# Performance work log

Hardware: AMD Instinct MI355X
Metric: run time of the kernel (lower is better)

Reference implementation:

```python
import jax, jax.numpy as jnp
import numpy as np

C = 128   # channels / dim
NH = 4    # num heads
HD = C // NH
K = 5     # conv kernel size: t=int((log2(128)+1)/2)=4 -> k=5
P = 12    # patch size
GH = 8    # grid height/width (96/12)
NPATCH = GH * GH
FEAT = P * P * C


def _ln(x, g, b):
    m = jnp.mean(x, -1, keepdims=True)
    v = jnp.var(x, -1, keepdims=True)
    return (x - m) / jnp.sqrt(v + 1e-5) * g + b


def _conv1d(x, w, pad):
    return jax.lax.conv_general_dilated(x, w, (1,), [(pad, pad)], dimension_numbers=('NCH', 'OIH', 'NCH'))


def _pool(x, out):
    # exact adaptive avg pool when H % out == 0
    B, c, H, W = x.shape
    f = H // out
    return x.reshape(B, c, out, f, out, f).mean((3, 5))


def _bilinear_ac(x, out):
    # bilinear interpolate [B,C,H,H] -> [B,C,out,out], align_corners=True
    H = x.shape[2]
    cpos = jnp.arange(out) * (H - 1) / (out - 1)
    i0 = jnp.floor(cpos).astype(jnp.int32)
    i1 = jnp.minimum(i0 + 1, H - 1)
    w = (cpos - i0).astype(x.dtype)
    xh = x[:, :, i0, :] * (1 - w)[None, None, :, None] + x[:, :, i1, :] * w[None, None, :, None]
    return xh[:, :, :, i0] * (1 - w) + xh[:, :, :, i1] * w


def setup_inputs() -> dict:
    key = jax.random.key(0)
    ks = jax.random.split(key, 8)
    B = 16
    return {
        's1': jax.random.normal(ks[0], (B, C, 96, 96), jnp.float32),
        'o': jax.random.normal(ks[1], (B, C, 64, 64), jnp.float32),
        'index': jax.random.randint(ks[2], (4, 2), 0, 96),
        'pe_w': jax.random.normal(ks[3], (64, 64, K), jnp.float32) * 0.05,
        'bn_g': jnp.ones((64,), jnp.float32),
        'bn_b': jnp.zeros((64,), jnp.float32),
        'bn_m': jnp.zeros((64,), jnp.float32),
        'bn_v': jnp.ones((64,), jnp.float32),
        'lnx_g': jnp.ones((C,), jnp.float32),
        'lnx_b': jnp.zeros((C,), jnp.float32),
        'lny_g': jnp.ones((C,), jnp.float32),
        'lny_b': jnp.zeros((C,), jnp.float32),
        'qkv_w': jax.random.normal(ks[4], (3 * C, C), jnp.float32) * 0.02,
        'qkv_b': jnp.zeros((3 * C,), jnp.float32),
        'yv_w': jax.random.normal(ks[5], (C, C), jnp.float32) * 0.02,
        'yv_b': jnp.zeros((C,), jnp.float32),
        'proj_w': jax.random.normal(ks[6], (C, C), jnp.float32) * 0.02,
        'proj_b': jnp.zeros((C,), jnp.float32),
        'c1d_w': jax.random.normal(ks[7], (C, C, K), jnp.float32) * 0.05,
    }


def reference(s1, o, index, pe_w, bn_g, bn_b, bn_m, bn_v, lnx_g, lnx_b, lny_g, lny_b,
              qkv_w, qkv_b, yv_w, yv_b, proj_w, proj_b, c1d_w):
    B = s1.shape[0]
    pad = (K - 1) // 2
    # --- mask(s1): patch embedding, conv1d+BN(eval)+ReLU, selective-square mask ---
    # einops: b c (h p1) (w p2) -> b (h w) (p1 p2 c)
    x = s1.reshape(B, C, GH, P, GH, P).transpose(0, 2, 4, 3, 5, 1).reshape(B, NPATCH, FEAT)
    x = _conv1d(x, pe_w, pad)
    x = (x - bn_m[None, :, None]) / jnp.sqrt(bn_v + 1e-5)[None, :, None] * bn_g[None, :, None] + bn_b[None, :, None]
    x = jax.nn.relu(x)
    # mask: rows at center indices keep value (mul by 1), all other rows squared
    idxs = index[:, 0] // P * GH + index[:, 1] // P
    sel = jnp.zeros((NPATCH,), bool).at[idxs].set(True)
    x = x * jnp.where(sel[None, :, None], 1.0, x)
    # einops back: b (h w) (p1 p2 c) -> b c (h p1) (w p2), then pool to 32
    x = x.reshape(B, GH, GH, P, P, C).transpose(0, 5, 1, 3, 2, 4).reshape(B, C, 96, 96)
    short = _pool(x, 32)                                   # [B,C,32,32]
    # --- attention branch ---
    op = _pool(o, 32)
    N = 32 * 32
    of = _ln(op.reshape(B, C, N).transpose(0, 2, 1), lnx_g, lnx_b)   # [B,N,C]
    ori = short.reshape(B, C, N).transpose(0, 2, 1)
    sn = _ln(ori, lny_g, lny_b)
    qkv = (of @ qkv_w.T + qkv_b).reshape(B, N, 3, NH, HD).transpose(2, 0, 3, 1, 4)
    q, k, v = qkv[0], qkv[1], qkv[2]                       # each [B,H,N,D]
    yv = (sn @ yv_w.T + yv_b).reshape(B, N, NH, HD).transpose(0, 2, 1, 3)
    attn = jax.nn.softmax(jnp.einsum('bhnd,bhmd->bhnm', q, k) * HD ** -0.5, axis=-1)
    xv = v + jnp.einsum('bhnm,bhmd->bhnd', attn, yv)
    xv = xv.transpose(0, 2, 1, 3).reshape(B, N, C) @ proj_w.T + proj_b
    xv = (xv + ori).transpose(0, 2, 1)                     # [B,C,N]
    xv = xv + _conv1d(xv, c1d_w, pad)
    xv = xv.reshape(B, C, 32, 32)
    return _bilinear_ac(xv, 96)
```

## Files before the change

kernel.cpp:

```cpp
#include <hip/hip_runtime.h>

#define FEAT 18432

typedef __attribute__((ext_vector_type(8))) short short8;
typedef __attribute__((ext_vector_type(4))) float f32x4;

__device__ __forceinline__ float b2f(unsigned short s) {
  union { unsigned int u; float f; } v; v.u = ((unsigned int)s) << 16; return v.f;
}
__device__ __forceinline__ unsigned short f2bf(float x) {
  union { float f; unsigned int u; } v; v.f = x;
  unsigned int u = v.u;
  unsigned int r = (u + 0x7FFFu + ((u >> 16) & 1u)) >> 16;
  return (unsigned short)r;
}

__device__ __forceinline__ void gl_lds16(const void* g, void* l) {
  __builtin_amdgcn_global_load_lds(
      (const __attribute__((address_space(1))) unsigned int*)g,
      (__attribute__((address_space(3))) unsigned int*)l, 16, 0, 0);
}

__global__ __launch_bounds__(256) void k_transpose(const float* __restrict__ s1,
                                                   unsigned short* __restrict__ xT) {
  int c = blockIdx.x, b = blockIdx.y;
  __shared__ float lds[96 * 99];
  int t = threadIdx.x;
  const float* src = s1 + ((size_t)b * 128 + c) * 9216;
  for (int idx = t; idx < 2304; idx += 256) {
    float4 v = ((const float4*)src)[idx];
    int h = idx / 24, w0 = (idx - h * 24) * 4;
    float* p = lds + h * 99 + w0;
    p[0] = v.x; p[1] = v.y; p[2] = v.z; p[3] = v.w;
  }
  __syncthreads();
  unsigned short* dstb = xT + (size_t)b * FEAT * 64;
  int sw = c & 7;
  for (int idx = t; idx < 1152; idx += 256) {
    int p1p2 = idx >> 3, gh = idx & 7;
    int p1 = p1p2 / 12, p2 = p1p2 - p1 * 12;
    const float* row = lds + (gh * 12 + p1) * 99 + p2;
    uint4 u;
    u.x = f2bf(row[0])  | ((unsigned int)f2bf(row[12]) << 16);
    u.y = f2bf(row[24]) | ((unsigned int)f2bf(row[36]) << 16);
    u.z = f2bf(row[48]) | ((unsigned int)f2bf(row[60]) << 16);
    u.w = f2bf(row[72]) | ((unsigned int)f2bf(row[84]) << 16);
    int f = p1p2 * 128 + c;
    int pos = gh ^ sw;
    *(uint4*)(dstb + (size_t)f * 64 + pos * 8) = u;
  }
}

__global__ __launch_bounds__(256) void k_prep(const float* __restrict__ pe_w,
                                              unsigned short* __restrict__ wpk) {
  int oc0 = blockIdx.x * 8;
  for (int e = threadIdx.x; e < 2560; e += 256) {
    int oc = oc0 + e / 320;
    int kL = e - (e / 320) * 320;
    int ic = kL & 63, kk = kL >> 6;
    float v = pe_w[(oc * 64 + ic) * 5 + kk];
    int LC = kL >> 3;
    int pos = (LC & 56) | ((LC & 7) ^ (oc & 7));
    wpk[oc * 320 + (pos << 3) + (kL & 7)] = f2bf(v);
  }
}

__global__ __launch_bounds__(256) void k_prepcw(const float* __restrict__ cw,
                                                unsigned short* __restrict__ wch) {
  int e = blockIdx.x * 256 + threadIdx.x;
  int oc = e / 640, kl = e - (e / 640) * 640;
  int kk = kl >> 7, ic = kl & 127;
  float v = cw[(size_t)oc * 640 + ic * 5 + kk];
  int LC = kl >> 3;
  int pos = (LC & 120) | ((LC & 7) ^ (oc & 7));
  wch[(size_t)oc * 640 + pos * 8 + (kl & 7)] = f2bf(v);
}

__global__ __launch_bounds__(256) void k_prepw(const float* __restrict__ W,
                                               unsigned short* __restrict__ dst,
                                               int ncols) {
  int idx = blockIdx.x * 256 + threadIdx.x;
  if (idx >= ncols * 16) return;
  int n = idx >> 4, c = idx & 15;
  int slot = (c & 8) | ((c & 7) ^ (n & 7));
  const float* s = W + (size_t)n * 128 + c * 8;
  uint4 u;
  u.x = (unsigned int)f2bf(s[0]) | ((unsigned int)f2bf(s[1]) << 16);
  u.y = (unsigned int)f2bf(s[2]) | ((unsigned int)f2bf(s[3]) << 16);
  u.z = (unsigned int)f2bf(s[4]) | ((unsigned int)f2bf(s[5]) << 16);
  u.w = (unsigned int)f2bf(s[6]) | ((unsigned int)f2bf(s[7]) << 16);
  *(uint4*)(dst + (size_t)n * 128 + slot * 8) = u;
}

__global__ __launch_bounds__(256) void k_conv_pe(
    const unsigned short* __restrict__ xT, const unsigned short* __restrict__ wpk,
    const float* __restrict__ bn_g, const float* __restrict__ bn_b,
    const float* __restrict__ bn_m, const float* __restrict__ bn_v,
    const int* __restrict__ indexp, unsigned short* __restrict__ ym) {
  extern __shared__ char smem[];
  unsigned short* Wl = (unsigned short*)smem;
  unsigned short* xl = (unsigned short*)(smem + 40960);
  float* scf = (float*)(smem + 74240);
  float* shf = (float*)(smem + 74496);
  int*   sli = (int*)(smem + 74752);
  int t = threadIdx.x;
  int b = blockIdx.y;
  int blk_f0 = blockIdx.x << 9;
  int lane = t & 63, w = t >> 6;
  int n16 = lane & 15, q = lane >> 4;

  for (int j = 0; j < 10; ++j) {
    int seg = w * 10 + j;
    gl_lds16((const char*)wpk + (seg << 10) + lane * 16, (char*)Wl + (seg << 10));
  }
  if (t < 64) {
    float sc = bn_g[t] * rsqrtf(bn_v[t] + 1e-5f);
    scf[t] = sc;
    shf[t] = bn_b[t] - bn_m[t] * sc;
    int i0 = indexp[0] / 12 * 8 + indexp[1] / 12;
    int i1 = indexp[2] / 12 * 8 + indexp[3] / 12;
    int i2 = indexp[4] / 12 * 8 + indexp[5] / 12;
    int i3 = indexp[6] / 12 * 8 + indexp[7] / 12;
    sli[t] = (t == i0 || t == i1 || t == i2 || t == i3) ? 1 : 0;
  }

  const unsigned short* xb = xT + (size_t)b * FEAT * 64;
  const unsigned int* xbu = (const unsigned int*)xb;

  for (int wnd = 0; wnd < 2; ++wnd) {
    int F0 = blk_f0 + (wnd << 8);
    __syncthreads();
    int flA = (F0 == 0) ? 2 : 0;
    for (int j = 0; j < 8; ++j) {
      int seg = (w << 3) + j;
      int gRow = F0 - 2 + flA + (seg << 3);
      gl_lds16((const char*)xb + (size_t)gRow * 128 + lane * 16,
               (char*)xl + flA * 128 + (seg << 10));
    }
    if (t < 128) {
      int r0 = (flA == 2) ? 0 : 256;
      int fl = (t < 64) ? (r0 + (t >> 5)) : (258 + ((t >> 5) & 1));
      int j = t & 31;
      int f = F0 - 2 + fl;
      unsigned int v = 0;
      if (f >= 0 && f < FEAT) v = xbu[(size_t)f * 32 + j];
      ((unsigned int*)xl)[fl * 32 + j] = v;
    }
    __syncthreads();

    f32x4 acc[4][4];
#pragma unroll
    for (int mt = 0; mt < 4; ++mt)
#pragma unroll
      for (int nt = 0; nt < 4; ++nt) acc[mt][nt] = (f32x4){0.f, 0.f, 0.f, 0.f};

    int rowB = w * 64 + n16;
#pragma unroll
    for (int kk = 0; kk < 5; ++kk) {
      int swb = (n16 + kk + 6) & 7;
#pragma unroll
      for (int ih = 0; ih < 2; ++ih) {
        int ca = (ih << 2) | q;
        const unsigned short* Ap = Wl + kk * 64 + ((ca ^ (n16 & 7)) << 3) + n16 * 320;
        short8 a0 = *(const short8*)(Ap);
        short8 a1 = *(const short8*)(Ap + 16 * 320);
        short8 a2 = *(const short8*)(Ap + 32 * 320);
        short8 a3 = *(const short8*)(Ap + 48 * 320);
        const unsigned short* Bp = xl + ((ca ^ swb) << 3) + (rowB + kk) * 64;
        short8 b0 = *(const short8*)(Bp);
        short8 b1 = *(const short8*)(Bp + 16 * 64);
        short8 b2 = *(const short8*)(Bp + 32 * 64);
        short8 b3 = *(const short8*)(Bp + 48 * 64);
        acc[0][0] = __builtin_amdgcn_mfma_f32_16x16x32_bf16(a0, b0, acc[0][0], 0, 0, 0);
        acc[0][1] = __builtin_amdgcn_mfma_f32_16x16x32_bf16(a0, b1, acc[0][1], 0, 0, 0);
// ... 53 lines not shown
#pragma unroll
    for (int dy = 0; dy < 3; ++dy)
#pragma unroll
      for (int dx = 0; dx < 3; ++dx)
        s += b2f(src[pbase + (dy * 12 + dx) * 128]);
    float val = s * (1.f / 9.f);
    float su = val, q = val * val;
#pragma unroll
    for (int off = 32; off > 0; off >>= 1) {
      su += __shfl_xor(su, off, 64);
      q += __shfl_xor(q, off, 64);
    }
    if (l64 == 0) { red[wv * 2] = su; red[wv * 2 + 1] = q; }
    __syncthreads();
    float S = red[hr * 4 + 0] + red[hr * 4 + 2];
    float Q = red[hr * 4 + 1] + red[hr * 4 + 3];
    float mean = S * (1.f / 128.f);
    float var = Q * (1.f / 128.f) - mean * mean;
    float inv = rsqrtf(var + 1e-5f);
    int n = (oh0 + pg1) * 32 + ow0 + pg2;
    size_t base = ((size_t)b * 1024 + n) * 128;
    ori[base + c] = val;
    float lnv = (val - mean) * inv * g + bb;
    int ch = c >> 3;
    int slot = (ch & 8) | ((ch & 7) ^ (n & 7));
    snh[base + slot * 8 + (c & 7)] = f2bf(lnv);
    __syncthreads();
  }
}

__global__ __launch_bounds__(256) void k_poolo_ln(
    const float* __restrict__ o, const float* __restrict__ lng,
    const float* __restrict__ lnb, unsigned short* __restrict__ oflh) {
  int y = blockIdx.x, b = blockIdx.y;
  __shared__ float pl[128 * 33];
  int t = threadIdx.x;
  for (int idx = t; idx < 4096; idx += 256) {
    int xo = idx & 31, c = idx >> 5;
    const float* p = o + (((size_t)b * 128 + c) * 64 + 2 * y) * 64 + 2 * xo;
    float2 a = *(const float2*)p;
    float2 d = *(const float2*)(p + 64);
    pl[c * 33 + xo] = 0.25f * (a.x + a.y + d.x + d.y);
  }
  __syncthreads();
  int xo = t >> 3, l8 = t & 7;
  float v[16]; float s = 0.f, q = 0.f;
#pragma unroll
  for (int i = 0; i < 16; ++i) {
    float x = pl[(l8 * 16 + i) * 33 + xo];
    v[i] = x; s += x; q += x * x;
  }
#pragma unroll
  for (int off = 1; off < 8; off <<= 1) {
    s += __shfl_xor(s, off, 8);
    q += __shfl_xor(q, off, 8);
  }
  float mean = s * (1.f / 128.f);
  float var = q * (1.f / 128.f) - mean * mean;
  float inv = rsqrtf(var + 1e-5f);
  int n = y * 32 + xo;
  unsigned short* dst = oflh + ((size_t)b * 1024 + n) * 128;
  int m7 = n & 7;
#pragma unroll
  for (int h = 0; h < 2; ++h) {
    int c = l8 * 2 + h;
    int slot = (c & 8) | ((c & 7) ^ m7);
    uint4 u;
    float w0 = (v[h * 8 + 0] - mean) * inv * lng[c * 8 + 0] + lnb[c * 8 + 0];
    float w1 = (v[h * 8 + 1] - mean) * inv * lng[c * 8 + 1] + lnb[c * 8 + 1];
    float w2 = (v[h * 8 + 2] - mean) * inv * lng[c * 8 + 2] + lnb[c * 8 + 2];
    float w3 = (v[h * 8 + 3] - mean) * inv * lng[c * 8 + 3] + lnb[c * 8 + 3];
    float w4 = (v[h * 8 + 4] - mean) * inv * lng[c * 8 + 4] + lnb[c * 8 + 4];
    float w5 = (v[h * 8 + 5] - mean) * inv * lng[c * 8 + 5] + lnb[c * 8 + 5];
    float w6 = (v[h * 8 + 6] - mean) * inv * lng[c * 8 + 6] + lnb[c * 8 + 6];
    float w7 = (v[h * 8 + 7] - mean) * inv * lng[c * 8 + 7] + lnb[c * 8 + 7];
    u.x = (unsigned int)f2bf(w0) | ((unsigned int)f2bf(w1) << 16);
    u.y = (unsigned int)f2bf(w2) | ((unsigned int)f2bf(w3) << 16);
    u.z = (unsigned int)f2bf(w4) | ((unsigned int)f2bf(w5) << 16);
    u.w = (unsigned int)f2bf(w6) | ((unsigned int)f2bf(w7) << 16);
    *(uint4*)(dst + slot * 8) = u;
  }
}

__global__ __launch_bounds__(256) void k_gemm_mfma(
    const unsigned short* __restrict__ A, const unsigned short* __restrict__ W,
    const float* __restrict__ bias, float* __restrict__ out, int Ncols) {
  __shared__ unsigned short Al[128 * 128];
  __shared__ unsigned short Bl[64 * 128];
  int m0 = blockIdx.x << 7, n0 = blockIdx.y << 6;
  int t = threadIdx.x;
  int lane = t & 63, w = t >> 6;
  int n16 = lane & 15, q = lane >> 4;

  for (int j = 0; j < 8; ++j) {
    int seg = w * 8 + j;
    gl_lds16((const char*)A + (size_t)m0 * 256 + (seg << 10) + lane * 16,
             (char*)Al + (seg << 10));
  }
  for (int j = 0; j < 4; ++j) {
    int seg = w * 4 + j;
    gl_lds16((const char*)W + (size_t)n0 * 256 + (seg << 10) + lane * 16,
             (char*)Bl + (seg << 10));
  }
  __syncthreads();

  int wm = w >> 1, wn = w & 1;
  f32x4 acc[4][2];
#pragma unroll
  for (int mt = 0; mt < 4; ++mt)
#pragma unroll
    for (int nt = 0; nt < 2; ++nt) acc[mt][nt] = (f32x4){0.f, 0.f, 0.f, 0.f};

#pragma unroll
  for (int kf = 0; kf < 4; ++kf) {
    int ca = kf * 4 + q;
    int rA0 = wm * 64 + n16;
    const unsigned short* Ap0 = Al + (size_t)rA0 * 128;
    int slotA = (ca & 8) | ((ca & 7) ^ (rA0 & 7));
    short8 a0 = *(const short8*)(Ap0 + slotA * 8);
    short8 a1 = *(const short8*)(Ap0 + 16 * 128 + slotA * 8);
    short8 a2 = *(const short8*)(Ap0 + 32 * 128 + slotA * 8);
    short8 a3 = *(const short8*)(Ap0 + 48 * 128 + slotA * 8);
    int rB0 = wn * 32 + n16;
    const unsigned short* Bp0 = Bl + (size_t)rB0 * 128;
    int slotB = (ca & 8) | ((ca & 7) ^ (rB0 & 7));
    short8 b0 = *(const short8*)(Bp0 + slotB * 8);
    short8 b1 = *(const short8*)(Bp0 + 16 * 128 + slotB * 8);
    acc[0][0] = __builtin_amdgcn_mfma_f32_16x16x32_bf16(a0, b0, acc[0][0], 0, 0, 0);
    acc[0][1] = __builtin_amdgcn_mfma_f32_16x16x32_bf16(a0, b1, acc[0][1], 0, 0, 0);
    acc[1][0] = __builtin_amdgcn_mfma_f32_16x16x32_bf16(a1, b0, acc[1][0], 0, 0, 0);
    acc[1][1] = __builtin_amdgcn_mfma_f32_16x16x32_bf16(a1, b1, acc[1][1], 0, 0, 0);
    acc[2][0] = __builtin_amdgcn_mfma_f32_16x16x32_bf16(a2, b0, acc[2][0], 0, 0, 0);
    acc[2][1] = __builtin_amdgcn_mfma_f32_16x16x32_bf16(a2, b1, acc[2][1], 0, 0, 0);
    acc[3][0] = __builtin_amdgcn_mfma_f32_16x16x32_bf16(a3, b0, acc[3][0], 0, 0, 0);
    acc[3][1] = __builtin_amdgcn_mfma_f32_16x16x32_bf16(a3, b1, acc[3][1], 0, 0, 0);
  }

#pragma unroll
  for (int mt = 0; mt < 4; ++mt) {
#pragma unroll
    for (int i = 0; i < 4; ++i) {
      int m = m0 + wm * 64 + mt * 16 + q * 4 + i;
#pragma unroll
      for (int nt = 0; nt < 2; ++nt) {
        int n = n0 + wn * 32 + nt * 16 + n16;
        out[(size_t)m * Ncols + n] = acc[mt][nt][i] + bias[n];
      }
    }
  }
}

__global__ __launch_bounds__(256) void k_proj_mfma(
    const unsigned short* __restrict__ A, const unsigned short* __restrict__ W,
    const float* __restrict__ bias, const float* __restrict__ ori,
    float* __restrict__ xv2, unsigned short* __restrict__ xph) {
  __shared__ unsigned short Al[128 * 128];
  __shared__ unsigned short Bl[64 * 128];
  int m0 = blockIdx.x << 7, n0 = blockIdx.y << 6;
  int t = threadIdx.x;
  int lane = t & 63, w = t >> 6;
  int n16 = lane & 15, q = lane >> 4;

  for (int j = 0; j < 8; ++j) {
    int seg = w * 8 + j;
    gl_lds16((const char*)A + (size_t)m0 * 256 + (seg << 10) + lane * 16,
             (char*)Al + (seg << 10));
  }
  for (int j = 0; j < 4; ++j) {
    int seg = w * 4 + j;
    gl_lds16((const char*)W + (size_t)n0 * 256 + (seg << 10) + lane * 16,
             (char*)Bl + (seg << 10));
  }
  __syncthreads();

  int wm = w >> 1, wn = w & 1;
  f32x4 acc[4][2];
#pragma unroll
  for (int mt = 0; mt < 4; ++mt)
#pragma unroll
    for (int nt = 0; nt < 2; ++nt) acc[mt][nt] = (f32x4){0.f, 0.f, 0.f, 0.f};

#pragma unroll
  for (int kf = 0; kf < 4; ++kf) {
    int ca = kf * 4 + q;
    int rA0 = wm * 64 + n16;
    const unsigned short* Ap0 = Al + (size_t)rA0 * 128;
    int slotA = (ca & 8) | ((ca & 7) ^ (rA0 & 7));
    short8 a0 = *(const short8*)(Ap0 + slotA * 8);
    short8 a1 = *(const short8*)(Ap0 + 16 * 128 + slotA * 8);
    short8 a2 = *(const short8*)(Ap0 + 32 * 128 + slotA * 8);
    short8 a3 = *(const short8*)(Ap0 + 48 * 128 + slotA * 8);
    int rB0 = wn * 32 + n16;
    const unsigned short* Bp0 = Bl + (size_t)rB0 * 128;
    int slotB = (ca & 8) | ((ca & 7) ^ (rB0 & 7));
    short8 b0 = *(const short8*)(Bp0 + slotB * 8);
    short8 b1 = *(const short8*)(Bp0 + 16 * 128 + slotB * 8);
    acc[0][0] = __builtin_amdgcn_mfma_f32_16x16x32_bf16(a0, b0, acc[0][0], 0, 0, 0);
    acc[0][1] = __builtin_amdgcn_mfma_f32_16x16x32_bf16(a0, b1, acc[0][1], 0, 0, 0);
    acc[1][0] = __builtin_amdgcn_mfma_f32_16x16x32_bf16(a1, b0, acc[1][0], 0, 0, 0);
    acc[1][1] = __builtin_amdgcn_mfma_f32_16x16x32_bf16(a1, b1, acc[1][1], 0, 0, 0);
    acc[2][0] = __builtin_amdgcn_mfma_f32_16x16x32_bf16(a2, b0, acc[2][0], 0, 0, 0);
    acc[2][1] = __builtin_amdgcn_mfma_f32_16x16x32_bf16(a2, b1, acc[2][1], 0, 0, 0);
    acc[3][0] = __builtin_amdgcn_mfma_f32_16x16x32_bf16(a3, b0, acc[3][0], 0, 0, 0);
    acc[3][1] = __builtin_amdgcn_mfma_f32_16x16x32_bf16(a3, b1, acc[3][1], 0, 0, 0);
  }

  int bb = m0 >> 10;
  int nbase = (m0 & 1023) + wm * 64;
#pragma unroll
  for (int mt = 0; mt < 4; ++mt) {
    int nloc = nbase + mt * 16 + q * 4;
    const float* orow = ori + ((size_t)bb * 1024 + nloc) * 128;
#pragma unroll
    for (int nt = 0; nt < 2; ++nt) {
      int c = n0 + wn * 32 + nt * 16 + n16;
      float pb = bias[c];
      float4 vv;
      vv.x = acc[mt][nt][0] + pb + orow[c];
      vv.y = acc[mt][nt][1] + pb + orow[128 + c];
      vv.z = acc[mt][nt][2] + pb + orow[256 + c];
      vv.w = acc[mt][nt][3] + pb + orow[384 + c];
      *(float4*)(xv2 + ((size_t)bb * 128 + c) * 1024 + nloc) = vv;
      int ch = c >> 3, ce = c & 7;
#pragma unroll
      for (int i = 0; i < 4; ++i) {
        int nrow = nloc + i;
        int slot = (ch & 8) | ((ch & 7) ^ (nrow & 7));
        float val = (i == 0) ? vv.x : (i == 1) ? vv.y : (i == 2) ? vv.z : vv.w;
        xph[((size_t)bb * 1024 + nrow) * 128 + slot * 8 + ce] = f2bf(val);
      }
    }
  }
}

__global__ __launch_bounds__(256) void k_cvt(const float* __restrict__ qkv,
                                             const float* __restrict__ yv,
                                             unsigned short* __restrict__ qkb,
                                             unsigned short* __restrict__ vtb) {
  int nt = blockIdx.x, b = blockIdx.y;
  int n0 = nt << 6;
  int t = threadIdx.x;
  __shared__ unsigned short tl[64 * 132];
  const float* qb = qkv + ((size_t)b * 1024 + n0) * 384;
  for (int it = 0; it < 16; ++it) {
    int idx = it * 256 + t;
    int n = idx >> 6, c4 = idx & 63;
    float4 v = *(const float4*)(qb + (size_t)n * 384 + c4 * 4);
    int c = c4 << 2;
    int kind = c >> 7, h = (c >> 5) & 3, d = c & 31;
    uint2 u;
    u.x = (unsigned int)f2bf(v.x) | ((unsigned int)f2bf(v.y) << 16);
    u.y = (unsigned int)f2bf(v.z) | ((unsigned int)f2bf(v.w) << 16);
    *(uint2*)(qkb + ((((size_t)b * 4 + h) * 2 + kind) * 1024 + n0 + n) * 32 + d) = u;
  }
  const float* vb = yv + ((size_t)b * 1024 + n0) * 128;
  for (int it = 0; it < 8; ++it) {
    int idx = it * 256 + t;
    int n = idx >> 5, c4 = idx & 31;
    float4 v = *(const float4*)(vb + (size_t)n * 128 + c4 * 4);
    unsigned short* o = tl + n * 132 + c4 * 4;
    o[0] = f2bf(v.x); o[1] = f2bf(v.y); o[2] = f2bf(v.z); o[3] = f2bf(v.w);
  }
  __syncthreads();
  int c = t >> 1, half = t & 1;
  unsigned short* orow = vtb + (((size_t)b * 4 + (c >> 5)) * 32 + (c & 31)) * 1024 + n0 + half * 32;
#pragma unroll
  for (int k = 0; k < 4; ++k) {
    short8 pack;
#pragma unroll
    for (int j = 0; j < 8; ++j)
      pack[j] = (short)tl[(half * 32 + k * 8 + j) * 132 + c];
    *(short8*)(orow + k * 8) = pack;
  }
}

__global__ __launch_bounds__(256) void k_attn(const float* __restrict__ qkv,
                                              const unsigned short* __restrict__ qkb,
                                              const unsigned short* __restrict__ vtb,
                                              unsigned short* __restrict__ atth) {
  int qt = blockIdx.x, h = blockIdx.y, b = blockIdx.z;
  __shared__ unsigned short Qs[64 * 40];
  __shared__ unsigned short Ks[128 * 40];
  __shared__ unsigned short Vt[32 * 136];
  __shared__ unsigned short Pw[4 * 16 * 136];
  int t = threadIdx.x;
  int lane = t & 63, w = t >> 6;
  int quad = lane >> 4, l16 = lane & 15;
  const float* qbase = qkv + (size_t)b * 1024 * 384;
  const unsigned short* qrow = qkb + (((size_t)b * 4 + h) * 2 + 0) * 1024 * 32;
  const unsigned short* krow = qkb + (((size_t)b * 4 + h) * 2 + 1) * 1024 * 32;
  const unsigned short* vrow = vtb + ((size_t)b * 4 + h) * 32 * 1024;
  int q0 = qt << 6;
  int hd = h * 32;

  {
    int r = t >> 2, cq = t & 3;
    short8 v = *(const short8*)(qrow + (size_t)(q0 + r) * 32 + cq * 8);
    *(short8*)(Qs + r * 40 + cq * 8) = v;
  }
  __syncthreads();
  short8 aq = *(const short8*)(Qs + (w * 16 + l16) * 40 + quad * 8);

  f32x4 O[2];
  O[0] = (f32x4){0.f, 0.f, 0.f, 0.f};
  O[1] = (f32x4){0.f, 0.f, 0.f, 0.f};
  float mi0 = -1e30f, li0 = 0.f;
  unsigned short* Pme = Pw + w * (16 * 136);
  const float scl = 0.17677669529663688f;

  for (int ci = 0; ci < 8; ++ci) {
    __syncthreads();
    int kn0 = ci << 7;
#pragma unroll
    for (int it = 0; it < 2; ++it) {
      int idx = it * 256 + t;
      int r = idx >> 2, cq = idx & 3;
      short8 kv = *(const short8*)(krow + (size_t)(kn0 + r) * 32 + cq * 8);
      *(short8*)(Ks + r * 40 + cq * 8) = kv;
      int d = idx >> 4, cc = idx & 15;
      short8 vv = *(const short8*)(vrow + (size_t)d * 1024 + kn0 + cc * 8);
      *(short8*)(Vt + d * 136 + cc * 8) = vv;
    }
    __syncthreads();

    f32x4 S[8];
#pragma unroll
    for (int nt = 0; nt < 8; ++nt) S[nt] = (f32x4){0.f, 0.f, 0.f, 0.f};
    __builtin_amdgcn_s_setprio(1);
#pragma unroll
    for (int nt = 0; nt < 8; ++nt) {
      short8 bk = *(const short8*)(Ks + (nt * 16 + l16) * 40 + quad * 8);
      S[nt] = __builtin_amdgcn_mfma_f32_16x16x32_bf16(bk, aq, S[nt], 0, 0, 0);
    }
    __builtin_amdgcn_s_setprio(0);

    float mg[8];
#pragma unroll
    for (int nt = 0; nt < 8; ++nt)
      mg[nt] = fmaxf(fmaxf(S[nt][0], S[nt][1]), fmaxf(S[nt][2], S[nt][3]));
    float rmr = fmaxf(fmaxf(fmaxf(mg[0], mg[1]), fmaxf(mg[2], mg[3])),
                      fmaxf(fmaxf(mg[4], mg[5]), fmaxf(mg[6], mg[7])));
    float rm = rmr * scl;
    rm = fmaxf(rm, __shfl_xor(rm, 16));
    rm = fmaxf(rm, __shfl_xor(rm, 32));
    float nm = fmaxf(mi0, rm);
    float alpha = __expf(mi0 - nm);
    mi0 = nm;

    float pstot = 0.f;
    unsigned short* pwr = Pme + l16 * 136 + quad * 4;
#pragma unroll
    for (int nt = 0; nt < 8; ++nt) {
      float p0 = __expf(S[nt][0] * scl - nm);
      float p1 = __expf(S[nt][1] * scl - nm);
      float p2 = __expf(S[nt][2] * scl - nm);
      float p3 = __expf(S[nt][3] * scl - nm);
      pstot += (p0 + p1) + (p2 + p3);
      uint2 u;
      u.x = (unsigned int)f2bf(p0) | ((unsigned int)f2bf(p1) << 16);
      u.y = (unsigned int)f2bf(p2) | ((unsigned int)f2bf(p3) << 16);
      *(uint2*)(pwr + nt * 16) = u;
    }
    float ps = pstot;
    ps += __shfl_xor(ps, 16);
    ps += __shfl_xor(ps, 32);
    li0 = li0 * alpha + ps;

    float al0 = __shfl(alpha, quad * 4 + 0);
    float al1 = __shfl(alpha, quad * 4 + 1);
    float al2 = __shfl(alpha, quad * 4 + 2);
    float al3 = __shfl(alpha, quad * 4 + 3);
    O[0][0] *= al0; O[1][0] *= al0;
    O[0][1] *= al1; O[1][1] *= al1;
    O[0][2] *= al2; O[1][2] *= al2;
    O[0][3] *= al3; O[1][3] *= al3;

    __builtin_amdgcn_s_setprio(1);
#pragma unroll
    for (int kc = 0; kc < 4; ++kc) {
      short8 bv0 = *(const short8*)(Vt + l16 * 136 + kc * 32 + quad * 8);
      short8 bv1 = *(const short8*)(Vt + (16 + l16) * 136 + kc * 32 + quad * 8);
      short8 ap = *(const short8*)(Pme + l16 * 136 + kc * 32 + quad * 8);
      O[0] = __builtin_amdgcn_mfma_f32_16x16x32_bf16(ap, bv0, O[0], 0, 0, 0);
      O[1] = __builtin_amdgcn_mfma_f32_16x16x32_bf16(ap, bv1, O[1], 0, 0, 0);
    }
    __builtin_amdgcn_s_setprio(0);
  }

#pragma unroll
  for (int reg = 0; reg < 4; ++reg) {
    float lit = __shfl(li0, quad * 4 + reg);
    int n = q0 + w * 16 + quad * 4 + reg;
    float inv = 1.f / lit;
    size_t mrow = ((size_t)b * 1024 + n) * 128;
    int m7 = n & 7;
#pragma unroll
    for (int nt = 0; nt < 2; ++nt) {
      int dd = hd + nt * 16 + l16;
      float val = O[nt][reg] * inv + qbase[(size_t)n * 384 + 256 + dd];
      int ch = dd >> 3;
      int slot = (ch & 8) | ((ch & 7) ^ m7);
      atth[mrow + slot * 8 + (dd & 7)] = f2bf(val);
    }
  }
}

__global__ __launch_bounds__(256) void k_conv1d_mfma(
    const unsigned short* __restrict__ xph, const unsigned short* __restrict__ wch,
    const float* __restrict__ xv2, float* __restrict__ xv3) {
  extern __shared__ char cs[];
  unsigned short* Wl = (unsigned short*)cs;
  unsigned short* xl = (unsigned short*)(cs + 81920);
  int ntile = blockIdx.x, b = blockIdx.y, oh = blockIdx.z;
  int n0 = ntile << 7;
  int t = threadIdx.x, lane = t & 63, w = t >> 6;
  int n16 = lane & 15, q = lane >> 4;

  const unsigned short* wsrc = wch + (size_t)oh * 64 * 640;
  for (int j = 0; j < 20; ++j) {
    int seg = w * 20 + j;
    gl_lds16((const char*)wsrc + (seg << 10) + lane * 16, (char*)Wl + (seg << 10));
  }
  const unsigned short* xpb = xph + (size_t)b * 1024 * 128;
  for (int j = 0; j < 8; ++j) {
    int seg = w * 8 + j;
    gl_lds16((const char*)xpb + (size_t)n0 * 256 + (seg << 10) + lane * 16,
             (char*)xl + 512 + (seg << 10));
  }
  {
    int ri = t >> 6, j2 = t & 63;
    int j = (ri < 2) ? ri : (128 + ri);
    int n = n0 + j - 2;
    unsigned int v = 0;
    if (n >= 0 && n < 1024) v = ((const unsigned int*)xpb)[(size_t)n * 64 + j2];
    ((unsigned int*)xl)[j * 64 + j2] = v;
  }
  __syncthreads();

  f32x4 acc[4][2];
#pragma unroll
  for (int mt = 0; mt < 4; ++mt)
#pragma unroll
    for (int nt = 0; nt < 2; ++nt) acc[mt][nt] = (f32x4){0.f, 0.f, 0.f, 0.f};

  int nb = w * 32;
#pragma unroll
  for (int kk = 0; kk < 5; ++kk) {
    int swb = (n16 + kk + 6) & 7;
#pragma unroll
    for (int kf = 0; kf < 4; ++kf) {
      int ca = kf * 4 + q;
      int LC = kk * 16 + kf * 4 + q;
      int slotA = (LC & 120) | ((LC & 7) ^ (n16 & 7));
      const unsigned short* Ap = Wl + n16 * 640 + slotA * 8;
      short8 a0 = *(const short8*)(Ap);
      short8 a1 = *(const short8*)(Ap + 16 * 640);
      short8 a2 = *(const short8*)(Ap + 32 * 640);
      short8 a3 = *(const short8*)(Ap + 48 * 640);
      int slotB = (ca & 8) | ((ca & 7) ^ swb);
      const unsigned short* Bp = xl + (nb + n16 + kk) * 128 + slotB * 8;
      short8 b0 = *(const short8*)(Bp);
      short8 b1 = *(const short8*)(Bp + 16 * 128);
      acc[0][0] = __builtin_amdgcn_mfma_f32_16x16x32_bf16(a0, b0, acc[0][0], 0, 0, 0);
      acc[0][1] = __builtin_amdgcn_mfma_f32_16x16x32_bf16(a0, b1, acc[0][1], 0, 0, 0);
      acc[1][0] = __builtin_amdgcn_mfma_f32_16x16x32_bf16(a1, b0, acc[1][0], 0, 0, 0);
      acc[1][1] = __builtin_amdgcn_mfma_f32_16x16x32_bf16(a1, b1, acc[1][1], 0, 0, 0);
      acc[2][0] = __builtin_amdgcn_mfma_f32_16x16x32_bf16(a2, b0, acc[2][0], 0, 0, 0);
      acc[2][1] = __builtin_amdgcn_mfma_f32_16x16x32_bf16(a2, b1, acc[2][1], 0, 0, 0);
      acc[3][0] = __builtin_amdgcn_mfma_f32_16x16x32_bf16(a3, b0, acc[3][0], 0, 0, 0);
      acc[3][1] = __builtin_amdgcn_mfma_f32_16x16x32_bf16(a3, b1, acc[3][1], 0, 0, 0);
    }
  }

#pragma unroll
  for (int mt = 0; mt < 4; ++mt) {
#pragma unroll
    for (int i = 0; i < 4; ++i) {
      int oc = oh * 64 + mt * 16 + q * 4 + i;
      const float* res = xv2 + ((size_t)b * 128 + oc) * 1024;
      float* outp = xv3 + ((size_t)b * 128 + oc) * 1024;
#pragma unroll
      for (int nt = 0; nt < 2; ++nt) {
        int n = n0 + nb + nt * 16 + n16;
        outp[n] = acc[mt][nt][i] + res[n];
      }
    }
  }
}

__global__ __launch_bounds__(256) void k_bilinear(const float* __restrict__ xv3,
                                                  float* __restrict__ out) {
  int idx = blockIdx.x * 256 + threadIdx.x;
  int X = idx % 96;
  int t2 = idx / 96;
  int Y = t2 % 96;
  int bc = t2 / 96;
  const float* src = xv3 + (size_t)bc * 1024;
  const float r = 31.f / 95.f;
  float py = Y * r, px = X * r;
  int y0 = (int)py, x0 = (int)px;
  float wy = py - y0, wx = px - x0;
  int y1 = y0 < 31 ? y0 + 1 : 31, x1 = x0 < 31 ? x0 + 1 : 31;
  float a = src[y0 * 32 + x0], b_ = src[y0 * 32 + x1];
  float c_ = src[y1 * 32 + x0], d_ = src[y1 * 32 + x1];
  float t0 = a * (1.f - wy) + c_ * wy;
  float t1 = b_ * (1.f - wy) + d_ * wy;
  out[idx] = t0 * (1.f - wx) + t1 * wx;
}

extern "C" void kernel_launch(void* const* d_in, const int* in_sizes, int n_in,
                              void* d_out, int out_size, void* d_ws, size_t ws_size,
                              hipStream_t stream) {
  (void)in_sizes; (void)n_in; (void)out_size; (void)ws_size;
  const float* s1    = (const float*)d_in[0];
  const float* o     = (const float*)d_in[1];
  const int*   indx  = (const int*)d_in[2];
  const float* pe_w  = (const float*)d_in[3];
  const float* bn_g  = (const float*)d_in[4];
  const float* bn_b  = (const float*)d_in[5];
  const float* bn_m  = (const float*)d_in[6];
  const float* bn_v  = (const float*)d_in[7];
  const float* lnx_g = (const float*)d_in[8];
  const float* lnx_b = (const float*)d_in[9];
  const float* lny_g = (const float*)d_in[10];
  const float* lny_b = (const float*)d_in[11];
  const float* qkv_w = (const float*)d_in[12];
  const float* qkv_b = (const float*)d_in[13];
  const float* yv_w  = (const float*)d_in[14];
  const float* yv_b  = (const float*)d_in[15];
  const float* proj_w = (const float*)d_in[16];
  const float* proj_b = (const float*)d_in[17];
  const float* c1d_w  = (const float*)d_in[18];

  char* ws = (char*)d_ws;
  unsigned short* xTh = (unsigned short*)ws;
  unsigned short* ymh = (unsigned short*)(ws + 37748736);
  unsigned short* wpk = (unsigned short*)d_out;
  unsigned short* wch = (unsigned short*)((char*)d_out + 65536);
  unsigned short* wqkh = (unsigned short*)((char*)d_out + 458752);
  unsigned short* wyvh = (unsigned short*)((char*)d_out + 573440);
  unsigned short* wprh = (unsigned short*)((char*)d_out + 622592);
  float* ori  = (float*)ws;
  unsigned short* snh  = (unsigned short*)(ws + 8388608);
  unsigned short* oflh = (unsigned short*)(ws + 16777216);
  unsigned short* atth = (unsigned short*)(ws + 25165824);
  float* qkvb  = (float*)(ws + 37748736);
  float* yvbuf = (float*)(ws + 62914560);
  unsigned short* qkb = (unsigned short*)(ws + 16777216);
  unsigned short* vtb = (unsigned short*)(ws + 71303168);
  float* xv2   = (float*)(ws + 37748736);
  float* xv3   = (float*)(ws + 46137344);
  unsigned short* xph = (unsigned short*)(ws + 62914560);

  hipLaunchKernelGGL(k_prep, dim3(8), dim3(256), 0, stream, pe_w, wpk);
  hipLaunchKernelGGL(k_prepcw, dim3(320), dim3(256), 0, stream, c1d_w, wch);
  hipLaunchKernelGGL(k_prepw, dim3(24), dim3(256), 0, stream, qkv_w, wqkh, 384);
  hipLaunchKernelGGL(k_prepw, dim3(8), dim3(256), 0, stream, yv_w, wyvh, 128);
  hipLaunchKernelGGL(k_prepw, dim3(8), dim3(256), 0, stream, proj_w, wprh, 128);
  hipLaunchKernelGGL(k_transpose, dim3(128, 16), dim3(256), 0, stream, s1, xTh);
  hipLaunchKernelGGL(k_conv_pe, dim3(36, 16), dim3(256), 75008, stream,
                     xTh, wpk, bn_g, bn_b, bn_m, bn_v, indx, ymh);
  hipLaunchKernelGGL(k_pool9ln, dim3(64, 16), dim3(256), 0, stream, ymh, lny_g, lny_b, ori, snh);
  hipLaunchKernelGGL(k_poolo_ln, dim3(32, 16), dim3(256), 0, stream, o, lnx_g, lnx_b, oflh);
  hipLaunchKernelGGL(k_gemm_mfma, dim3(128, 6), dim3(256), 0, stream, oflh, wqkh, qkv_b, qkvb, 384);
  hipLaunchKernelGGL(k_gemm_mfma, dim3(128, 2), dim3(256), 0, stream, snh, wyvh, yv_b, yvbuf, 128);
  hipLaunchKernelGGL(k_cvt, dim3(16, 16), dim3(256), 0, stream, qkvb, yvbuf, qkb, vtb);
  hipLaunchKernelGGL(k_attn, dim3(16, 4, 16), dim3(256), 0, stream, qkvb, qkb, vtb, atth);
  hipLaunchKernelGGL(k_proj_mfma, dim3(128, 2), dim3(256), 0, stream, atth, wprh, proj_b, ori, xv2, xph);
  hipLaunchKernelGGL(k_conv1d_mfma, dim3(8, 16, 2), dim3(256), 115712, stream, xph, wch, xv2, xv3);
  hipLaunchKernelGGL(k_bilinear, dim3(73728), dim3(256), 0, stream, xv3, (float*)d_out);
}
```

Baseline: 345.6 us.

## Fuse bf16 conversion into QKV/YV GEMM epilogues and merge weight prep kernels

The QKV and YV GEMMs now write their results directly in the bf16 head-major layouts that attention consumes (Q/K packed per head, YV transposed per head), and V is written as a separate fp32 residual buffer. This removes the k_cvt kernel and its fp32 round trip through memory. The five weight-prep kernels are merged into one launch to cut launch overhead. In exchange, the epilogue stores become scattered 2-byte writes, which may coalesce poorly, and the workspace buffers are reassigned.

```diff
diff --git a/kernel.cpp b/kernel.cpp
--- a/kernel.cpp
+++ b/kernel.cpp
@@ -3,6 +3,7 @@
 #define FEAT 18432
 
 typedef __attribute__((ext_vector_type(8))) short short8;
+typedef __attribute__((ext_vector_type(4))) short short4t;
 typedef __attribute__((ext_vector_type(4))) float f32x4;
 
 __device__ __forceinline__ float b2f(unsigned short s) {
@@ -51,35 +52,10 @@
   }
 }
 
-__global__ __launch_bounds__(256) void k_prep(const float* __restrict__ pe_w,
-                                              unsigned short* __restrict__ wpk) {
-  int oc0 = blockIdx.x * 8;
-  for (int e = threadIdx.x; e < 2560; e += 256) {
-    int oc = oc0 + e / 320;
-    int kL = e - (e / 320) * 320;
-    int ic = kL & 63, kk = kL >> 6;
-    float v = pe_w[(oc * 64 + ic) * 5 + kk];
-    int LC = kL >> 3;
-    int pos = (LC & 56) | ((LC & 7) ^ (oc & 7));
-    wpk[oc * 320 + (pos << 3) + (kL & 7)] = f2bf(v);
-  }
-}
-
-__global__ __launch_bounds__(256) void k_prepcw(const float* __restrict__ cw,
-                                                unsigned short* __restrict__ wch) {
-  int e = blockIdx.x * 256 + threadIdx.x;
-  int oc = e / 640, kl = e - (e / 640) * 640;
-  int kk = kl >> 7, ic = kl & 127;
-  float v = cw[(size_t)oc * 640 + ic * 5 + kk];
-  int LC = kl >> 3;
-  int pos = (LC & 120) | ((LC & 7) ^ (oc & 7));
-  wch[(size_t)oc * 640 + pos * 8 + (kl & 7)] = f2bf(v);
-}
-
-__global__ __launch_bounds__(256) void k_prepw(const float* __restrict__ W,
-                                               unsigned short* __restrict__ dst,
-                                               int ncols) {
-  int idx = blockIdx.x * 256 + threadIdx.x;
+__device__ __forceinline__ void prepw_body(const float* __restrict__ W,
+                                           unsigned short* __restrict__ dst,
+                                           int ncols, int bx, int t) {
+  int idx = bx * 256 + t;
   if (idx >= ncols * 16) return;
   int n = idx >> 4, c = idx & 15;
   int slot = (c & 8) | ((c & 7) ^ (n & 7));
@@ -90,6 +66,41 @@
   u.z = (unsigned int)f2bf(s[4]) | ((unsigned int)f2bf(s[5]) << 16);
   u.w = (unsigned int)f2bf(s[6]) | ((unsigned int)f2bf(s[7]) << 16);
   *(uint4*)(dst + (size_t)n * 128 + slot * 8) = u;
+}
+
+__global__ __launch_bounds__(256) void k_prepall(
+    const float* __restrict__ pe_w, unsigned short* __restrict__ wpk,
+    const float* __restrict__ cw, unsigned short* __restrict__ wch,
+    const float* __restrict__ qkv_w, unsigned short* __restrict__ wqkh,
+    const float* __restrict__ yv_w, unsigned short* __restrict__ wyvh,
+    const float* __restrict__ proj_w, unsigned short* __restrict__ wprh) {
+  int bx = blockIdx.x, t = threadIdx.x;
+  if (bx < 8) {
+    int oc0 = bx * 8;
+    for (int e = t; e < 2560; e += 256) {
+      int oc = oc0 + e / 320;
+      int kL = e - (e / 320) * 320;
+      int ic = kL & 63, kk = kL >> 6;
+      float v = pe_w[(oc * 64 + ic) * 5 + kk];
+      int LC = kL >> 3;
+      int pos = (LC & 56) | ((LC & 7) ^ (oc & 7));
+      wpk[oc * 320 + (pos << 3) + (kL & 7)] = f2bf(v);
+    }
+  } else if (bx < 328) {
+    int e = (bx - 8) * 256 + t;
+    int oc = e / 640, kl = e - (e / 640) * 640;
+    int kk = kl >> 7, ic = kl & 127;
+    float v = cw[(size_t)oc * 640 + ic * 5 + kk];
+    int LC = kl >> 3;
+    int pos = (LC & 120) | ((LC & 7) ^ (oc & 7));
+    wch[(size_t)oc * 640 + pos * 8 + (kl & 7)] = f2bf(v);
+  } else if (bx < 352) {
+    prepw_body(qkv_w, wqkh, 384, bx - 328, t);
+  } else if (bx < 360) {
+    prepw_body(yv_w, wyvh, 128, bx - 352, t);
+  } else {
+    prepw_body(proj_w, wprh, 128, bx - 360, t);
+  }
 }
 
 __global__ __launch_bounds__(256) void k_conv_pe(
@@ -309,70 +320,110 @@
   }
 }
 
-__global__ __launch_bounds__(256) void k_gemm_mfma(
+#define GEMM_CORE()                                                              \
+  for (int j = 0; j < 8; ++j) {                                                  \
+    int seg = w * 8 + j;                                                         \
+    gl_lds16((const char*)A + (size_t)m0 * 256 + (seg << 10) + lane * 16,        \
+             (char*)Al + (seg << 10));                                           \
+  }                                                                              \
+  for (int j = 0; j < 4; ++j) {                                                  \
+    int seg = w * 4 + j;                                                         \
+    gl_lds16((const char*)W + (size_t)n0 * 256 + (seg << 10) + lane * 16,        \
+             (char*)Bl + (seg << 10));                                           \
+  }                                                                              \
+  __syncthreads();                                                               \
+  int wm = w >> 1, wn = w & 1;                                                   \
+  f32x4 acc[4][2];                                                               \
+  _Pragma("unroll")                                                              \
+  for (int mt = 0; mt < 4; ++mt)                                                 \
+    _Pragma("unroll")                                                            \
+    for (int nt = 0; nt < 2; ++nt) acc[mt][nt] = (f32x4){0.f, 0.f, 0.f, 0.f};    \
+  _Pragma("unroll")                                                              \
+  for (int kf = 0; kf < 4; ++kf) {                                               \
+    int ca = kf * 4 + q;                                                         \
+    int rA0 = wm * 64 + n16;                                                     \
+    const unsigned short* Ap0 = Al + (size_t)rA0 * 128;                          \
+    int slotA = (ca & 8) | ((ca & 7) ^ (rA0 & 7));                               \
+    short8 a0 = *(const short8*)(Ap0 + slotA * 8);                               \
+    short8 a1 = *(const short8*)(Ap0 + 16 * 128 + slotA * 8);                    \
+    short8 a2 = *(const short8*)(Ap0 + 32 * 128 + slotA * 8);                    \
+    short8 a3 = *(const short8*)(Ap0 + 48 * 128 + slotA * 8);                    \
+    int rB0 = wn * 32 + n16;                                                     \
+    const unsigned short* Bp0 = Bl + (size_t)rB0 * 128;                          \
+    int slotB = (ca & 8) | ((ca & 7) ^ (rB0 & 7));                               \
+    short8 b0 = *(const short8*)(Bp0 + slotB * 8);                               \
+    short8 b1 = *(const short8*)(Bp0 + 16 * 128 + slotB * 8);                    \
+    acc[0][0] = __builtin_amdgcn_mfma_f32_16x16x32_bf16(a0, b0, acc[0][0], 0, 0, 0); \
+    acc[0][1] = __builtin_amdgcn_mfma_f32_16x16x32_bf16(a0, b1, acc[0][1], 0, 0, 0); \
+    acc[1][0] = __builtin_amdgcn_mfma_f32_16x16x32_bf16(a1, b0, acc[1][0], 0, 0, 0); \
+    acc[1][1] = __builtin_amdgcn_mfma_f32_16x16x32_bf16(a1, b1, acc[1][1], 0, 0, 0); \
+    acc[2][0] = __builtin_amdgcn_mfma_f32_16x16x32_bf16(a2, b0, acc[2][0], 0, 0, 0); \
+    acc[2][1] = __builtin_amdgcn_mfma_f32_16x16x32_bf16(a2, b1, acc[2][1], 0, 0, 0); \
+    acc[3][0] = __builtin_amdgcn_mfma_f32_16x16x32_bf16(a3, b0, acc[3][0], 0, 0, 0); \
+    acc[3][1] = __builtin_amdgcn_mfma_f32_16x16x32_bf16(a3, b1, acc[3][1], 0, 0, 0); \
+  }
+
+__global__ __launch_bounds__(256) void k_gemm_qkv(
     const unsigned short* __restrict__ A, const unsigned short* __restrict__ W,
-    const float* __restrict__ bias, float* __restrict__ out, int Ncols) {
+    const float* __restrict__ bias, unsigned short* __restrict__ qkb,
+    float* __restrict__ vres) {
   __shared__ unsigned short Al[128 * 128];
   __shared__ unsigned short Bl[64 * 128];
   int m0 = blockIdx.x << 7, n0 = blockIdx.y << 6;
   int t = threadIdx.x;
   int lane = t & 63, w = t >> 6;
   int n16 = lane & 15, q = lane >> 4;
-
-  for (int j = 0; j < 8; ++j) {
-    int seg = w * 8 + j;
-    gl_lds16((const char*)A + (size_t)m0 * 256 + (seg << 10) + lane * 16,
-             (char*)Al + (seg << 10));
-  }
-  for (int j = 0; j < 4; ++j) {
-    int seg = w * 4 + j;
-    gl_lds16((const char*)W + (size_t)n0 * 256 + (seg << 10) + lane * 16,
-             (char*)Bl + (seg << 10));
-  }
-  __syncthreads();
-
-  int wm = w >> 1, wn = w & 1;
-  f32x4 acc[4][2];
-#pragma unroll
-  for (int mt = 0; mt < 4; ++mt)
-#pragma unroll
-    for (int nt = 0; nt < 2; ++nt) acc[mt][nt] = (f32x4){0.f, 0.f, 0.f, 0.f};
-
-#pragma unroll
-  for (int kf = 0; kf < 4; ++kf) {
-    int ca = kf * 4 + q;
-    int rA0 = wm * 64 + n16;
-    const unsigned short* Ap0 = Al + (size_t)rA0 * 128;
-    int slotA = (ca & 8) | ((ca & 7) ^ (rA0 & 7));
-    short8 a0 = *(const short8*)(Ap0 + slotA * 8);
-    short8 a1 = *(const short8*)(Ap0 + 16 * 128 + slotA * 8);
-    short8 a2 = *(const short8*)(Ap0 + 32 * 128 + slotA * 8);
-    short8 a3 = *(const short8*)(Ap0 + 48 * 128 + slotA * 8);
-    int rB0 = wn * 32 + n16;
-    const unsigned short* Bp0 = Bl + (size_t)rB0 * 128;
-    int slotB = (ca & 8) | ((ca & 7) ^ (rB0 & 7));
-    short8 b0 = *(const short8*)(Bp0 + slotB * 8);
-    short8 b1 = *(const short8*)(Bp0 + 16 * 128 + slotB * 8);
-    acc[0][0] = __builtin_amdgcn_mfma_f32_16x16x32_bf16(a0, b0, acc[0][0], 0, 0, 0);
-    acc[0][1] = __builtin_amdgcn_mfma_f32_16x16x32_bf16(a0, b1, acc[0][1], 0, 0, 0);
-    acc[1][0] = __builtin_amdgcn_mfma_f32_16x16x32_bf16(a1, b0, acc[1][0], 0, 0, 0);
-    acc[1][1] = __builtin_amdgcn_mfma_f32_16x16x32_bf16(a1, b1, acc[1][1], 0, 0, 0);
-    acc[2][0] = __builtin_amdgcn_mfma_f32_16x16x32_bf16(a2, b0, acc[2][0], 0, 0, 0);
-    acc[2][1] = __builtin_amdgcn_mfma_f32_16x16x32_bf16(a2, b1, acc[2][1], 0, 0, 0);
-    acc[3][0] = __builtin_amdgcn_mfma_f32_16x16x32_bf16(a3, b0, acc[3][0], 0, 0, 0);
-    acc[3][1] = __builtin_amdgcn_mfma_f32_16x16x32_bf16(a3, b1, acc[3][1], 0, 0, 0);
-  }
-
+  GEMM_CORE()
+
+  int bb = m0 >> 10;
+  int nbase = (m0 & 1023) + wm * 64;
 #pragma unroll
   for (int mt = 0; mt < 4; ++mt) {
 #pragma unroll
     for (int i = 0; i < 4; ++i) {
-      int m = m0 + wm * 64 + mt * 16 + q * 4 + i;
+      int nloc = nbase + mt * 16 + q * 4 + i;
 #pragma unroll
       for (int nt = 0; nt < 2; ++nt) {
         int n = n0 + wn * 32 + nt * 16 + n16;
-        out[(size_t)m * Ncols + n] = acc[mt][nt][i] + bias[n];
+        float val = acc[mt][nt][i] + bias[n];
+        if (n < 256) {
+          int kind = n >> 7, h = (n >> 5) & 3, d = n & 31;
+          qkb[((((size_t)bb * 4 + h) * 2 + kind) * 1024 + nloc) * 32 + d] = f2bf(val);
+        } else {
+          vres[((size_t)bb * 1024 + nloc) * 128 + (n - 256)] = val;
+        }
       }
+    }
+  }
+}
+
+__global__ __launch_bounds__(256) void k_gemm_yv(
+    const unsigned short* __restrict__ A, const unsigned short* __restrict__ W,
+    const float* __restrict__ bias, unsigned short* __restrict__ vtb) {
+  __shared__ unsigned short Al[128 * 128];
+  __shared__ unsigned short Bl[64 * 128];
+  int m0 = blockIdx.x << 7, n0 = blockIdx.y << 6;
+  int t = threadIdx.x;
+  int lane = t & 63, w = t >> 6;
+  int n16 = lane & 15, q = lane >> 4;
+  GEMM_CORE()
+
+  int bb = m0 >> 10;
+  int nbase = (m0 & 1023) + wm * 64;
+#pragma unroll
+  for (int mt = 0; mt < 4; ++mt) {
+    int nloc = nbase + mt * 16 + q * 4;
+#pragma unroll
+    for (int nt = 0; nt < 2; ++nt) {
+      int c = n0 + wn * 32 + nt * 16 + n16;
+      float pb = bias[c];
+      int h = c >> 5, d = c & 31;
+      short4t pk;
+      pk[0] = (short)f2bf(acc[mt][nt][0] + pb);
+      pk[1] = (short)f2bf(acc[mt][nt][1] + pb);
+      pk[2] = (short)f2bf(acc[mt][nt][2] + pb);
+      pk[3] = (short)f2bf(acc[mt][nt][3] + pb);
+      *(short4t*)(vtb + (((size_t)bb * 4 + h) * 32 + d) * 1024 + nloc) = pk;
     }
   }
 }
@@ -387,50 +438,7 @@
   int t = threadIdx.x;
   int lane = t & 63, w = t >> 6;
   int n16 = lane & 15, q = lane >> 4;
-
-  for (int j = 0; j < 8; ++j) {
-    int seg = w * 8 + j;
-    gl_lds16((const char*)A + (size_t)m0 * 256 + (seg << 10) + lane * 16,
-             (char*)Al + (seg << 10));
-  }
-  for (int j = 0; j < 4; ++j) {
-    int seg = w * 4 + j;
-    gl_lds16((const char*)W + (size_t)n0 * 256 + (seg << 10) + lane * 16,
-             (char*)Bl + (seg << 10));
-  }
-  __syncthreads();
-
-  int wm = w >> 1, wn = w & 1;
-  f32x4 acc[4][2];
-#pragma unroll
-  for (int mt = 0; mt < 4; ++mt)
-#pragma unroll
-    for (int nt = 0; nt < 2; ++nt) acc[mt][nt] = (f32x4){0.f, 0.f, 0.f, 0.f};
-
-#pragma unroll
-  for (int kf = 0; kf < 4; ++kf) {
-    int ca = kf * 4 + q;
-    int rA0 = wm * 64 + n16;
-    const unsigned short* Ap0 = Al + (size_t)rA0 * 128;
-    int slotA = (ca & 8) | ((ca & 7) ^ (rA0 & 7));
-    short8 a0 = *(const short8*)(Ap0 + slotA * 8);
-    short8 a1 = *(const short8*)(Ap0 + 16 * 128 + slotA * 8);
-    short8 a2 = *(const short8*)(Ap0 + 32 * 128 + slotA * 8);
-    short8 a3 = *(const short8*)(Ap0 + 48 * 128 + slotA * 8);
-    int rB0 = wn * 32 + n16;
-    const unsigned short* Bp0 = Bl + (size_t)rB0 * 128;
-    int slotB = (ca & 8) | ((ca & 7) ^ (rB0 & 7));
-    short8 b0 = *(const short8*)(Bp0 + slotB * 8);
-    short8 b1 = *(const short8*)(Bp0 + 16 * 128 + slotB * 8);
-    acc[0][0] = __builtin_amdgcn_mfma_f32_16x16x32_bf16(a0, b0, acc[0][0], 0, 0, 0);
-    acc[0][1] = __builtin_amdgcn_mfma_f32_16x16x32_bf16(a0, b1, acc[0][1], 0, 0, 0);
-    acc[1][0] = __builtin_amdgcn_mfma_f32_16x16x32_bf16(a1, b0, acc[1][0], 0, 0, 0);
-    acc[1][1] = __builtin_amdgcn_mfma_f32_16x16x32_bf16(a1, b1, acc[1][1], 0, 0, 0);
-    acc[2][0] = __builtin_amdgcn_mfma_f32_16x16x32_bf16(a2, b0, acc[2][0], 0, 0, 0);
-    acc[2][1] = __builtin_amdgcn_mfma_f32_16x16x32_bf16(a2, b1, acc[2][1], 0, 0, 0);
-    acc[3][0] = __builtin_amdgcn_mfma_f32_16x16x32_bf16(a3, b0, acc[3][0], 0, 0, 0);
-    acc[3][1] = __builtin_amdgcn_mfma_f32_16x16x32_bf16(a3, b1, acc[3][1], 0, 0, 0);
-  }
+  GEMM_CORE()
 
   int bb = m0 >> 10;
   int nbase = (m0 & 1023) + wm * 64;
@@ -460,48 +468,7 @@
   }
 }
 
-__global__ __launch_bounds__(256) void k_cvt(const float* __restrict__ qkv,
-                                             const float* __restrict__ yv,
-                                             unsigned short* __restrict__ qkb,
-                                             unsigned short* __restrict__ vtb) {
-  int nt = blockIdx.x, b = blockIdx.y;
-  int n0 = nt << 6;
-  int t = threadIdx.x;
-  __shared__ unsigned short tl[64 * 132];
-  const float* qb = qkv + ((size_t)b * 1024 + n0) * 384;
-  for (int it = 0; it < 16; ++it) {
-    int idx = it * 256 + t;
-    int n = idx >> 6, c4 = idx & 63;
-    float4 v = *(const float4*)(qb + (size_t)n * 384 + c4 * 4);
-    int c = c4 << 2;
-    int kind = c >> 7, h = (c >> 5) & 3, d = c & 31;
-    uint2 u;
-    u.x = (unsigned int)f2bf(v.x) | ((unsigned int)f2bf(v.y) << 16);
-    u.y = (unsigned int)f2bf(v.z) | ((unsigned int)f2bf(v.w) << 16);
-    *(uint2*)(qkb + ((((size_t)b * 4 + h) * 2 + kind) * 1024 + n0 + n) * 32 + d) = u;
-  }
-  const float* vb = yv + ((size_t)b * 1024 + n0) * 128;
-  for (int it = 0; it < 8; ++it) {
-    int idx = it * 256 + t;
-    int n = idx >> 5, c4 = idx & 31;
-    float4 v = *(const float4*)(vb + (size_t)n * 128 + c4 * 4);
-    unsigned short* o = tl + n * 132 + c4 * 4;
-    o[0] = f2bf(v.x); o[1] = f2bf(v.y); o[2] = f2bf(v.z); o[3] = f2bf(v.w);
-  }
-  __syncthreads();
-  int c = t >> 1, half = t & 1;
-  unsigned short* orow = vtb + (((size_t)b * 4 + (c >> 5)) * 32 + (c & 31)) * 1024 + n0 + half * 32;
-#pragma unroll
-  for (int k = 0; k < 4; ++k) {
-    short8 pack;
-#pragma unroll
-    for (int j = 0; j < 8; ++j)
-      pack[j] = (short)tl[(half * 32 + k * 8 + j) * 132 + c];
-    *(short8*)(orow + k * 8) = pack;
-  }
-}
-
-__global__ __launch_bounds__(256) void k_attn(const float* __restrict__ qkv,
+__global__ __launch_bounds__(256) void k_attn(const float* __restrict__ vres,
                                               const unsigned short* __restrict__ qkb,
                                               const unsigned short* __restrict__ vtb,
                                               unsigned short* __restrict__ atth) {
@@ -513,7 +480,6 @@
   int t = threadIdx.x;
   int lane = t & 63, w = t >> 6;
   int quad = lane >> 4, l16 = lane & 15;
-  const float* qbase = qkv + (size_t)b * 1024 * 384;
   const unsigned short* qrow = qkb + (((size_t)b * 4 + h) * 2 + 0) * 1024 * 32;
   const unsigned short* krow = qkb + (((size_t)b * 4 + h) * 2 + 1) * 1024 * 32;
   const unsigned short* vrow = vtb + ((size_t)b * 4 + h) * 32 * 1024;
@@ -624,7 +590,7 @@
 #pragma unroll
     for (int nt = 0; nt < 2; ++nt) {
       int dd = hd + nt * 16 + l16;
-      float val = O[nt][reg] * inv + qbase[(size_t)n * 384 + 256 + dd];
+      float val = O[nt][reg] * inv + vres[mrow + dd];
       int ch = dd >> 3;
       int slot = (ch & 8) | ((ch & 7) ^ m7);
       atth[mrow + slot * 8 + (dd & 7)] = f2bf(val);
@@ -771,28 +737,23 @@
   unsigned short* snh  = (unsigned short*)(ws + 8388608);
   unsigned short* oflh = (unsigned short*)(ws + 16777216);
   unsigned short* atth = (unsigned short*)(ws + 25165824);
-  float* qkvb  = (float*)(ws + 37748736);
-  float* yvbuf = (float*)(ws + 62914560);
-  unsigned short* qkb = (unsigned short*)(ws + 16777216);
-  unsigned short* vtb = (unsigned short*)(ws + 71303168);
-  float* xv2   = (float*)(ws + 37748736);
-  float* xv3   = (float*)(ws + 46137344);
-  unsigned short* xph = (unsigned short*)(ws + 62914560);
-
-  hipLaunchKernelGGL(k_prep, dim3(8), dim3(256), 0, stream, pe_w, wpk);
-  hipLaunchKernelGGL(k_prepcw, dim3(320), dim3(256), 0, stream, c1d_w, wch);
-  hipLaunchKernelGGL(k_prepw, dim3(24), dim3(256), 0, stream, qkv_w, wqkh, 384);
-  hipLaunchKernelGGL(k_prepw, dim3(8), dim3(256), 0, stream, yv_w, wyvh, 128);
-  hipLaunchKernelGGL(k_prepw, dim3(8), dim3(256), 0, stream, proj_w, wprh, 128);
+  float* vres = (float*)(ws + 37748736);
+  unsigned short* qkb = (unsigned short*)(ws + 46137344);
+  unsigned short* vtb = (unsigned short*)(ws + 54525952);
+  float* xv2 = (float*)(ws + 37748736);
+  unsigned short* xph = (unsigned short*)(ws + 46137344);
+  float* xv3 = (float*)(ws + 54525952);
+
+  hipLaunchKernelGGL(k_prepall, dim3(368), dim3(256), 0, stream,
+                     pe_w, wpk, c1d_w, wch, qkv_w, wqkh, yv_w, wyvh, proj_w, wprh);
   hipLaunchKernelGGL(k_transpose, dim3(128, 16), dim3(256), 0, stream, s1, xTh);
   hipLaunchKernelGGL(k_conv_pe, dim3(36, 16), dim3(256), 75008, stream,
                      xTh, wpk, bn_g, bn_b, bn_m, bn_v, indx, ymh);
   hipLaunchKernelGGL(k_pool9ln, dim3(64, 16), dim3(256), 0, stream, ymh, lny_g, lny_b, ori, snh);
   hipLaunchKernelGGL(k_poolo_ln, dim3(32, 16), dim3(256), 0, stream, o, lnx_g, lnx_b, oflh);
-  hipLaunchKernelGGL(k_gemm_mfma, dim3(128, 6), dim3(256), 0, stream, oflh, wqkh, qkv_b, qkvb, 384);
-  hipLaunchKernelGGL(k_gemm_mfma, dim3(128, 2), dim3(256), 0, stream, snh, wyvh, yv_b, yvbuf, 128);
-  hipLaunchKernelGGL(k_cvt, dim3(16, 16), dim3(256), 0, stream, qkvb, yvbuf, qkb, vtb);
-  hipLaunchKernelGGL(k_attn, dim3(16, 4, 16), dim3(256), 0, stream, qkvb, qkb, vtb, atth);
+  hipLaunchKernelGGL(k_gemm_qkv, dim3(128, 6), dim3(256), 0, stream, oflh, wqkh, qkv_b, qkb, vres);
+  hipLaunchKernelGGL(k_gemm_yv, dim3(128, 2), dim3(256), 0, stream, snh, wyvh, yv_b, vtb);
+  hipLaunchKernelGGL(k_attn, dim3(16, 4, 16), dim3(256), 0, stream, vres, qkb, vtb, atth);
   hipLaunchKernelGGL(k_proj_mfma, dim3(128, 2), dim3(256), 0, stream, atth, wprh, proj_b, ori, xv2, xph);
   hipLaunchKernelGGL(k_conv1d_mfma, dim3(8, 16, 2), dim3(256), 115712, stream, xph, wch, xv2, xv3);
   hipLaunchKernelGGL(k_bilinear, dim3(73728), dim3(256), 0, stream, xv3, (float*)d_out);
```

After: 330.9 us. 1.04x faster.
